# Performance work log

Hardware: AMD Instinct MI355X
Metric: run time of the kernel (lower is better)

## Reference

```python
import jax, jax.numpy as jnp
import numpy as np

D = 512
H = 8
DH = D // H


def setup_inputs() -> dict:
    key = jax.random.key(0)
    ks = jax.random.split(key, 6)
    B, S = 2, 4096
    scale = 1.0 / np.sqrt(D)
    x = jax.random.normal(ks[0], (B, S, D), dtype=jnp.float32)
    W_q = jax.random.normal(ks[1], (D, D), dtype=jnp.float32) * scale
    W_k = jax.random.normal(ks[2], (D, D), dtype=jnp.float32) * scale
    W_v = jax.random.normal(ks[3], (D, D), dtype=jnp.float32) * scale
    W_proj = jax.random.normal(ks[4], (D, D), dtype=jnp.float32) * scale
    b_proj = jax.random.normal(ks[5], (D,), dtype=jnp.float32) * 0.01
    return {"x": x, "W_q": W_q, "W_k": W_k, "W_v": W_v,
            "W_proj": W_proj, "b_proj": b_proj}


def reference(x, W_q, W_k, W_v, W_proj, b_proj):
    B, S, _ = x.shape
    # torch Linear: y = x @ W.T
    def proj(W):
        y = jnp.einsum('bsd,ed->bse', x, W)
        return y.reshape(B, S, H, DH).transpose(0, 2, 1, 3)  # [B,H,S,DH]
    q, k, v = proj(W_q), proj(W_k), proj(W_v)
    scores = jnp.einsum('bhqd,bhkd->bhqk', q, k) / np.sqrt(DH)  # [B,H,S,S]
    causal = jnp.tril(jnp.ones((S, S), dtype=bool))
    neg = jnp.finfo(scores.dtype).min
    scores = jnp.where(causal[None, None, :, :], scores, neg)
    w = jax.nn.softmax(scores, axis=-1)
    attn = jnp.einsum('bhqk,bhkd->bhqd', w, v)  # [B,H,S,DH]
    attn = attn.transpose(0, 2, 1, 3).reshape(B, S, D)
    return jnp.einsum('bsd,ed->bse', attn, W_proj) + b_proj
```

## Files before the change

### kernel.cpp

```cpp
#include <hip/hip_runtime.h>
#include <hip/hip_bf16.h>
#include <stdint.h>

#define D_MODEL 512
#define NH 8
#define DH 64
#define SEQ 4096
#define NBH 16
#define NX  (2 * SEQ * D_MODEL)
#define NW  (D_MODEL * D_MODEL)

typedef __attribute__((ext_vector_type(8))) short bf16x8;
typedef __attribute__((ext_vector_type(4))) float f32x4;
typedef __attribute__((ext_vector_type(16))) float f32x16;

#define CSCALE 0.18033688011112042f

__device__ __forceinline__ uint32_t pkbf(float a, float b) {
    uint32_t r;
    asm("v_cvt_pk_bf16_f32 %0, %1, %2" : "=v"(r) : "v"(a), "v"(b));
    return r;
}

#define SWZ(R) (((R) + ((R) >> 2)) & 3)

#define BAR() do {                                          \
    asm volatile("s_waitcnt lgkmcnt(0)" ::: "memory");      \
    __builtin_amdgcn_s_barrier();                           \
} while (0)

#define BARV() do {                                              \
    asm volatile("s_waitcnt vmcnt(0) lgkmcnt(0)" ::: "memory");  \
    __builtin_amdgcn_s_barrier();                                \
} while (0)

typedef const __attribute__((address_space(1))) void* gvp;
typedef __attribute__((address_space(3))) void* lvp;
__device__ __forceinline__ void gload16(const short* g, short* l) {
    __builtin_amdgcn_global_load_lds((gvp)g, (lvp)l, 16, 0, 0);
}

__device__ __forceinline__ bf16x8 cvt8(float4 u, float4 v, float s) {
    union { uint32_t w[4]; bf16x8 h; } r;
    r.w[0] = pkbf(u.x * s, u.y * s); r.w[1] = pkbf(u.z * s, u.w * s);
    r.w[2] = pkbf(v.x * s, v.y * s); r.w[3] = pkbf(v.z * s, v.w * s);
    return r.h;
}

__global__ __launch_bounds__(256) void cvt_pre(
    const float* __restrict__ x,
    const float* __restrict__ Wq, const float* __restrict__ Wk,
    const float* __restrict__ Wv, const float* __restrict__ Wp,
    short* __restrict__ xb, short* __restrict__ Wb)
{
    const size_t t = ((size_t)blockIdx.x * 256 + threadIdx.x) * 8;
    const float* src; short* dst; float s = 1.0f; size_t off;
    if (t < NX) {
        src = x; dst = xb; off = t;
    } else {
        const size_t u = t - NX;
        const int w = (int)(u >> 18);
        off = u & (NW - 1);
        src = (w == 0) ? Wq : (w == 1) ? Wk : (w == 2) ? Wv : Wp;
        dst = Wb + ((size_t)w << 18);
        s = (w == 0) ? CSCALE : 1.0f;
    }
    float4 a = *(const float4*)(src + off);
    float4 b = *(const float4*)(src + off + 4);
    *(bf16x8*)(dst + off) = cvt8(a, b, s);
}

__global__ __launch_bounds__(256) void qkv_kernel(
    const short* __restrict__ xb, const short* __restrict__ Wb,
    short* __restrict__ Qb, short* __restrict__ Kb, short* __restrict__ Vt)
{
    __shared__ __align__(16) short at[2][4096];
    __shared__ __align__(16) short bt[2][4096];

    const int tid  = threadIdx.x;
    const int wave = tid >> 6;
    const int lane = tid & 63;
    const int ln = lane & 15, quad = lane >> 4;
    const int z = blockIdx.z;
    const short* W = Wb + ((size_t)z << 18);
    const int m0 = blockIdx.x * 128;
    const int n0 = blockIdx.y * 128;
    const int mh = (wave & 1) * 64, nh = (wave >> 1) * 64;

    const int ck0 = tid, ck1 = tid + 256;
    const int R0 = ck0 >> 2, R1 = ck1 >> 2;
    const int c0 = (ck0 & 3) ^ SWZ(R0), c1 = (ck1 & 3) ^ SWZ(R1);
    const int lbase = (tid & 192) * 8;

    auto stage = [&](int buf, int kc) {
        const short* gA0 = xb + (size_t)(m0 + R0) * D_MODEL + kc + c0 * 8;
        const short* gA1 = xb + (size_t)(m0 + R1) * D_MODEL + kc + c1 * 8;
        const short* gB0 = W + (size_t)(n0 + R0) * D_MODEL + kc + c0 * 8;
        const short* gB1 = W + (size_t)(n0 + R1) * D_MODEL + kc + c1 * 8;
        gload16(gA0, &at[buf][lbase]);
        gload16(gA1, &at[buf][lbase] + 2048);
        gload16(gB0, &bt[buf][lbase]);
        gload16(gB1, &bt[buf][lbase] + 2048);
    };

    f32x4 acc[4][4] = {};

    stage(0, 0);

    for (int s = 0; s < 16; ++s) {
        const int cur = s & 1;
        BARV();
        if (s < 15) stage(cur ^ 1, (s + 1) * 32);

        bf16x8 a[4], b[4];
#pragma unroll
        for (int i = 0; i < 4; ++i) {
            const int R = mh + i * 16 + ln;
            a[i] = *(const bf16x8*)(&at[cur][R * 32 + ((quad ^ SWZ(R)) * 8)]);
        }
#pragma unroll
        for (int j = 0; j < 4; ++j) {
            const int R = nh + j * 16 + ln;
            b[j] = *(const bf16x8*)(&bt[cur][R * 32 + ((quad ^ SWZ(R)) * 8)]);
        }
        __builtin_amdgcn_s_setprio(1);
#pragma unroll
        for (int i = 0; i < 4; ++i)
#pragma unroll
            for (int j = 0; j < 4; ++j)
                acc[i][j] = __builtin_amdgcn_mfma_f32_16x16x32_bf16(
                    a[i], b[j], acc[i][j], 0, 0, 0);
        __builtin_amdgcn_s_setprio(0);
    }

    if (z == 2) {
#pragma unroll
        for (int i = 0; i < 4; ++i) {
            const int row0 = m0 + mh + i * 16 + quad * 4;
            const int bb = row0 >> 12, sq = row0 & (SEQ - 1);
#pragma unroll
            for (int j = 0; j < 4; ++j) {
                const int n = n0 + nh + j * 16 + ln;
                const int h = n >> 6, dh = n & 63;
                uint2 st;
                st.x = pkbf(acc[i][j][0], acc[i][j][1]);
                st.y = pkbf(acc[i][j][2], acc[i][j][3]);
                *(uint2*)(Vt + (size_t)((bb * NH + h) * DH + dh) * SEQ + sq) = st;
            }
        }
    } else {
        short* P = (z == 0) ? Qb : Kb;
#pragma unroll
        for (int i = 0; i < 4; ++i)
#pragma unroll
            for (int j = 0; j < 4; ++j) {
                const int n = n0 + nh + j * 16 + ln;
                const int h = n >> 6, dh = n & 63;
                const uint32_t lo = pkbf(acc[i][j][0], acc[i][j][1]);
                const uint32_t hi2 = pkbf(acc[i][j][2], acc[i][j][3]);
#pragma unroll
                for (int r = 0; r < 4; ++r) {
                    const int row = m0 + mh + i * 16 + quad * 4 + r;
                    const int bb = row >> 12, sq = row & (SEQ - 1);
                    const uint32_t w = (r < 2) ? lo : hi2;
                    P[((size_t)((bb * NH + h) * SEQ + sq) << 6) + dh] =
                        (short)((r & 1) ? (w >> 16) : (w & 0xffff));
                }
            }
    }
}

__global__ __launch_bounds__(256) void attn_kernel(
    const short* __restrict__ Qb, const short* __restrict__ Kb,
    const short* __restrict__ Vt, short* __restrict__ ao)
{
    __shared__ __align__(16) short kt[2][4096];
    __shared__ __align__(16) short vt[2][4096];

    const int tid  = threadIdx.x;
    const int wave = tid >> 6;
    const int lane = tid & 63;
    const int l31 = lane & 31, hi = lane >> 5;
    const int bh = blockIdx.y;
    const int w_ = (blockIdx.x + 4 * bh) & 31;
    const int g2 = ((bh >> 3) & 1) ? (31 - w_) : w_;
    const short* Qp = Qb + (size_t)bh * SEQ * DH;
    const short* Kp = Kb + (size_t)bh * SEQ * DH;
    const short* Vp = Vt + (size_t)bh * DH * SEQ;
    const int bb = bh >> 3, h = bh & 7;
    const int q0 = g2 * 128 + wave * 32;
    const int myq = q0 + l31;
    const int jdiag = q0 >> 6;
    const int jmax = 2 * g2 + 1;

    const int ckA = tid, ckB = tid + 256;
    const int RA = ckA >> 3, RB = ckB >> 3;
    const int cA = (ckA & 7) ^ (RA & 7), cB = (ckB & 7) ^ (RB & 7);
    const int RA31 = RA & 31, RB31 = RB & 31;
    const int kkA = (RA & 32) + ((RA31 & 8) << 1) + ((RA31 & 4) << 1)
                  + ((RA31 & 16) >> 2) + (RA31 & 3);
    const int kkB = (RB & 32) + ((RB31 & 8) << 1) + ((RB31 & 4) << 1)
                  + ((RB31 & 16) >> 2) + (RB31 & 3);
    const size_t kOffA = ((size_t)kkA << 6) + cA * 8;
    const size_t kOffB = ((size_t)kkB << 6) + cB * 8;
    const size_t vOffA = (size_t)RA * SEQ + cA * 8;
    const size_t vOffB = (size_t)RB * SEQ + cB * 8;

    bf16x8 sk0, sk1, sv0, sv1;
    auto load_tile = [&](int j) {
        const size_t k0 = (size_t)j * 64;
        sk0 = *(const bf16x8*)(Kp + (k0 << 6) + kOffA);
        sk1 = *(const bf16x8*)(Kp + (k0 << 6) + kOffB);
        sv0 = *(const bf16x8*)(Vp + vOffA + k0);
        sv1 = *(const bf16x8*)(Vp + vOffB + k0);
    };
    auto write_tile = [&](int buf) {
        *(bf16x8*)&kt[buf][ckA * 8] = sk0;
        *(bf16x8*)&kt[buf][ckB * 8] = sk1;
        *(bf16x8*)&vt[buf][ckA * 8] = sv0;
        *(bf16x8*)&vt[buf][ckB * 8] = sv1;
    };

    bf16x8 qf[4];
#pragma unroll
    for (int c = 0; c < 4; ++c)
        qf[c] = *(const bf16x8*)(Qp + (size_t)myq * DH + c * 16 + hi * 8);

    const bf16x8 ones = { (short)0x3F80, (short)0x3F80, (short)0x3F80,
                          (short)0x3F80, (short)0x3F80, (short)0x3F80,
                          (short)0x3F80, (short)0x3F80 };

    f32x16 o0 = {}, o1 = {};
    f32x16 lacc = {};

    load_tile(0);
    write_tile(0);
    load_tile(1);
    BAR();

    for (int j = 0; j <= jmax; ++j) {
        const int cur = j & 1;
        if (j < jmax) {
            write_tile(cur ^ 1);
            if (j + 1 < jmax) load_tile(j + 2);
        }

        if ((j << 6) <= q0 + 31) {
            f32x16 s0 = {}, s1 = {};
            const int sw = l31 & 7;
            __builtin_amdgcn_s_setprio(1);
#pragma unroll
            for (int c = 0; c < 4; ++c) {
                const int pc = ((2 * c + hi) ^ sw) * 8;
                bf16x8 a0 = *(const bf16x8*)(&kt[cur][l31 * 64 + pc]);
                bf16x8 a1 = *(const bf16x8*)(&kt[cur][(32 + l31) * 64 + pc]);
                s0 = __builtin_amdgcn_mfma_f32_32x32x16_bf16(a0, qf[c], s0, 0, 0, 0);
                s1 = __builtin_amdgcn_mfma_f32_32x32x16_bf16(a1, qf[c], s1, 0, 0, 0);
            }
            __builtin_amdgcn_s_setprio(0);
            if (j >= jdiag) {
                const int k0 = j * 64;
#pragma unroll
                for (int reg = 0; reg < 16; ++reg) {
                    const int kl = ((reg >> 2) & 1) * 16 + hi * 8
                                 + ((reg >> 3) & 1) * 4 + (reg & 3);
                    if (k0 + kl > myq)      s0[reg] = -3e38f;
                    if (k0 + 32 + kl > myq) s1[reg] = -3e38f;
                }
            }
#pragma unroll
            for (int i = 0; i < 16; ++i) {
                s0[i] = __builtin_amdgcn_exp2f(s0[i]);
                s1[i] = __builtin_amdgcn_exp2f(s1[i]);
            }

            union { uint32_t u[4]; bf16x8 v; } p00, p01, p10, p11;
            p00.u[0] = pkbf(s0[0], s0[1]);   p00.u[1] = pkbf(s0[2], s0[3]);
            p00.u[2] = pkbf(s0[8], s0[9]);   p00.u[3] = pkbf(s0[10], s0[11]);
            p01.u[0] = pkbf(s0[4], s0[5]);   p01.u[1] = pkbf(s0[6], s0[7]);
            p01.u[2] = pkbf(s0[12], s0[13]); p01.u[3] = pkbf(s0[14], s0[15]);
            p10.u[0] = pkbf(s1[0], s1[1]);   p10.u[1] = pkbf(s1[2], s1[3]);
            p10.u[2] = pkbf(s1[8], s1[9]);   p10.u[3] = pkbf(s1[10], s1[11]);
            p11.u[0] = pkbf(s1[4], s1[5]);   p11.u[1] = pkbf(s1[6], s1[7]);
            p11.u[2] = pkbf(s1[12], s1[13]); p11.u[3] = pkbf(s1[14], s1[15]);

            __builtin_amdgcn_s_setprio(1);
            lacc = __builtin_amdgcn_mfma_f32_32x32x16_bf16(ones, p00.v, lacc, 0, 0, 0);
            lacc = __builtin_amdgcn_mfma_f32_32x32x16_bf16(ones, p01.v, lacc, 0, 0, 0);
            lacc = __builtin_amdgcn_mfma_f32_32x32x16_bf16(ones, p10.v, lacc, 0, 0, 0);
            lacc = __builtin_amdgcn_mfma_f32_32x32x16_bf16(ones, p11.v, lacc, 0, 0, 0);

            {
                const short* vrow = &vt[cur][l31 * 64];
                bf16x8 v00 = *(const bf16x8*)(vrow + (((0 + hi) ^ sw) * 8));
                bf16x8 v01 = *(const bf16x8*)(vrow + (((2 + hi) ^ sw) * 8));
                bf16x8 v10 = *(const bf16x8*)(vrow + (((4 + hi) ^ sw) * 8));
                bf16x8 v11 = *(const bf16x8*)(vrow + (((6 + hi) ^ sw) * 8));
                o0 = __builtin_amdgcn_mfma_f32_32x32x16_bf16(v00, p00.v, o0, 0, 0, 0);
                o0 = __builtin_amdgcn_mfma_f32_32x32x16_bf16(v01, p01.v, o0, 0, 0, 0);
                o0 = __builtin_amdgcn_mfma_f32_32x32x16_bf16(v10, p10.v, o0, 0, 0, 0);
                o0 = __builtin_amdgcn_mfma_f32_32x32x16_bf16(v11, p11.v, o0, 0, 0, 0);
            }
            {
                const short* vrow = &vt[cur][(32 + l31) * 64];
                bf16x8 v00 = *(const bf16x8*)(vrow + (((0 + hi) ^ sw) * 8));
                bf16x8 v01 = *(const bf16x8*)(vrow + (((2 + hi) ^ sw) * 8));
                bf16x8 v10 = *(const bf16x8*)(vrow + (((4 + hi) ^ sw) * 8));
                bf16x8 v11 = *(const bf16x8*)(vrow + (((6 + hi) ^ sw) * 8));
                o1 = __builtin_amdgcn_mfma_f32_32x32x16_bf16(v00, p00.v, o1, 0, 0, 0);
                o1 = __builtin_amdgcn_mfma_f32_32x32x16_bf16(v01, p01.v, o1, 0, 0, 0);
                o1 = __builtin_amdgcn_mfma_f32_32x32x16_bf16(v10, p10.v, o1, 0, 0, 0);
                o1 = __builtin_amdgcn_mfma_f32_32x32x16_bf16(v11, p11.v, o1, 0, 0, 0);
            }
            __builtin_amdgcn_s_setprio(0);
        }
        BAR();
    }
    const float inv = 1.0f / lacc[0];
    short* orow = ao + (size_t)(bb * SEQ + myq) * D_MODEL + h * DH;
#pragma unroll
    for (int c = 0; c < 4; ++c) {
        uint2 st;
        st.x = pkbf(o0[4 * c] * inv,     o0[4 * c + 1] * inv);
        st.y = pkbf(o0[4 * c + 2] * inv, o0[4 * c + 3] * inv);
        *(uint2*)(orow + 8 * c + 4 * hi) = st;
    }
#pragma unroll
    for (int c = 0; c < 4; ++c) {
        uint2 st;
        st.x = pkbf(o1[4 * c] * inv,     o1[4 * c + 1] * inv);
        st.y = pkbf(o1[4 * c + 2] * inv, o1[4 * c + 3] * inv);
        *(uint2*)(orow + 32 + 8 * c + 4 * hi) = st;
    }
}

__global__ __launch_bounds__(256) void proj_kernel(
    const short* __restrict__ attn, const short* __restrict__ Wpb,
    const float* __restrict__ bias, float* __restrict__ out)
{
    __shared__ __align__(16) short at[2][2048];
    __shared__ __align__(16) short bt[2][4096];

    const int tid  = threadIdx.x;
    const int wave = tid >> 6;
    const int lane = tid & 63;
    const int ln = lane & 15, quad = lane >> 4;
    const int m0 = blockIdx.x * 64;
    const int n0 = blockIdx.y * 128;
    const int mh = (wave & 1) * 32, nh = (wave >> 1) * 64;

    const int RA = tid >> 2, cAc = (tid & 3) ^ SWZ(RA);
    const int ck0 = tid, ck1 = tid + 256;
    const int R0 = ck0 >> 2, R1 = ck1 >> 2;
    const int c0 = (ck0 & 3) ^ SWZ(R0), c1 = (ck1 & 3) ^ SWZ(R1);
    const int lbase = (tid & 192) * 8;

    auto stage = [&](int buf, int kc) {
        const short* gA = attn + (size_t)(m0 + RA) * D_MODEL + kc + cAc * 8;
        const short* gB0 = Wpb + (size_t)(n0 + R0) * D_MODEL + kc + c0 * 8;
        const short* gB1 = Wpb + (size_t)(n0 + R1) * D_MODEL + kc + c1 * 8;
        gload16(gA, &at[buf][lbase]);
        gload16(gB0, &bt[buf][lbase]);
        gload16(gB1, &bt[buf][lbase] + 2048);
    };

    f32x4 acc[2][4] = {};

    stage(0, 0);

    for (int s = 0; s < 16; ++s) {
        const int cur = s & 1;
        BARV();
        if (s < 15) stage(cur ^ 1, (s + 1) * 32);

        bf16x8 a[2], b[4];
#pragma unroll
        for (int i = 0; i < 2; ++i) {
            const int R = mh + i * 16 + ln;
            a[i] = *(const bf16x8*)(&at[cur][R * 32 + ((quad ^ SWZ(R)) * 8)]);
        }
#pragma unroll
        for (int j = 0; j < 4; ++j) {
            const int R = nh + j * 16 + ln;
            b[j] = *(const bf16x8*)(&bt[cur][R * 32 + ((quad ^ SWZ(R)) * 8)]);
        }
        __builtin_amdgcn_s_setprio(1);
#pragma unroll
        for (int i = 0; i < 2; ++i)
#pragma unroll
            for (int j = 0; j < 4; ++j)
                acc[i][j] = __builtin_amdgcn_mfma_f32_16x16x32_bf16(
                    a[i], b[j], acc[i][j], 0, 0, 0);
        __builtin_amdgcn_s_setprio(0);
    }
#pragma unroll
    for (int j = 0; j < 4; ++j) {
        const int n = n0 + nh + j * 16 + ln;
        const float bv = bias[n];
#pragma unroll
        for (int i = 0; i < 2; ++i)
#pragma unroll
            for (int r = 0; r < 4; ++r) {
                const int row = m0 + mh + i * 16 + quad * 4 + r;
                out[(size_t)row * D_MODEL + n] = acc[i][j][r] + bv;
            }
    }
}

extern "C" void kernel_launch(void* const* d_in, const int* in_sizes, int n_in,
                              void* d_out, int out_size, void* d_ws, size_t ws_size,
                              hipStream_t stream) {
    const float* x  = (const float*)d_in[0];
    const float* Wq = (const float*)d_in[1];
    const float* Wk = (const float*)d_in[2];
    const float* Wv = (const float*)d_in[3];
    const float* Wp = (const float*)d_in[4];
    const float* bp = (const float*)d_in[5];
    float* out = (float*)d_out;

    short* Qb = (short*)d_ws;
    short* Kb = Qb + (size_t)NBH * SEQ * DH;
    short* Vt = Kb + (size_t)NBH * SEQ * DH;
    short* ab = Vt + (size_t)NBH * SEQ * DH;
    short* Wb = ab + (size_t)NBH * SEQ * DH;

    short* xb = (short*)d_out;

    cvt_pre<<<dim3((NX + 4 * NW) / (8 * 256)), 256, 0, stream>>>(
        x, Wq, Wk, Wv, Wp, xb, Wb);
    qkv_kernel<<<dim3(64, 4, 3), 256, 0, stream>>>(xb, Wb, Qb, Kb, Vt);
    attn_kernel<<<dim3(32, NBH), 256, 0, stream>>>(Qb, Kb, Vt, ab);
    proj_kernel<<<dim3(128, 4), 256, 0, stream>>>(ab, Wb + 3 * (size_t)NW, bp, out);
}
```

Measured before the change: 168.6 us.

## Software-pipeline PV MFMAs across tiles and stage Q/K stores through LDS

The attention loop now defers the P·V and row-sum MFMAs of the previous key tile into the current iteration, so they issue alongside the QK^T MFMAs while the exp and pack of the current tile run afterward. V fragments are loaded into registers before the barrier so the next iteration can use them. Separately, the QKV projection epilogue for Q and K writes the tile into swizzled shared-memory scratch and then emits 16-byte coalesced row stores instead of scattered 2-byte global stores. This raises register pressure, since V and P fragments stay live across iterations, and adds an LDS round trip plus a barrier in the projection kernel.

Measured after the change: 181.2 us. +7.5%, slower.

```diff
diff --git a/kernel.cpp b/kernel.cpp
--- a/kernel.cpp
+++ b/kernel.cpp
@@ -150,23 +150,35 @@
         }
     } else {
         short* P = (z == 0) ? Qb : Kb;
+        BAR();
+        short* scratch = (wave < 2) ? &at[wave][0] : &bt[wave - 2][0];
 #pragma unroll
         for (int i = 0; i < 4; ++i)
 #pragma unroll
             for (int j = 0; j < 4; ++j) {
-                const int n = n0 + nh + j * 16 + ln;
-                const int h = n >> 6, dh = n & 63;
-                const uint32_t lo = pkbf(acc[i][j][0], acc[i][j][1]);
+                const uint32_t lo  = pkbf(acc[i][j][0], acc[i][j][1]);
                 const uint32_t hi2 = pkbf(acc[i][j][2], acc[i][j][3]);
+                const int lc = 16 * j + ln;
+                const int cw = lc & 7, ch = lc >> 3;
 #pragma unroll
                 for (int r = 0; r < 4; ++r) {
-                    const int row = m0 + mh + i * 16 + quad * 4 + r;
-                    const int bb = row >> 12, sq = row & (SEQ - 1);
+                    const int lr = 16 * i + 4 * quad + r;
                     const uint32_t w = (r < 2) ? lo : hi2;
-                    P[((size_t)((bb * NH + h) * SEQ + sq) << 6) + dh] =
+                    scratch[lr * 64 + ((ch ^ (lr & 7)) << 3) + cw] =
                         (short)((r & 1) ? (w >> 16) : (w & 0xffff));
                 }
             }
+        asm volatile("s_waitcnt lgkmcnt(0)" ::: "memory");
+        const int hh = (n0 + nh) >> 6;
+        const int rg = m0 + mh + lane;
+        const int bb2 = rg >> 12, sq2 = rg & (SEQ - 1);
+        short* dst = P + (((size_t)(bb2 * NH + hh) * SEQ + sq2) << 6);
+#pragma unroll
+        for (int c = 0; c < 8; ++c) {
+            const int swc = c ^ (lane & 7);
+            *(bf16x8*)(dst + 8 * c) =
+                *(const bf16x8*)&scratch[lane * 64 + swc * 8];
+        }
     }
 }
 
@@ -233,6 +245,10 @@
     f32x16 o0 = {}, o1 = {};
     f32x16 lacc = {};
 
+    bf16x8 vp0, vp1, vp2, vp3, vp4, vp5, vp6, vp7;
+    bf16x8 pp0, pp1, pp2, pp3;
+    bool havePrev = false;
+
     load_tile(0);
     write_tile(0);
     load_tile(1);
@@ -245,10 +261,12 @@
             if (j + 1 < jmax) load_tile(j + 2);
         }
 
-        if ((j << 6) <= q0 + 31) {
-            f32x16 s0 = {}, s1 = {};
-            const int sw = l31 & 7;
-            __builtin_amdgcn_s_setprio(1);
+        const bool comp = ((j << 6) <= q0 + 31);
+        f32x16 s0 = {}, s1 = {};
+        const int sw = l31 & 7;
+
+        __builtin_amdgcn_s_setprio(1);
+        if (comp) {
 #pragma unroll
             for (int c = 0; c < 4; ++c) {
                 const int pc = ((2 * c + hi) ^ sw) * 8;
@@ -257,7 +275,38 @@
                 s0 = __builtin_amdgcn_mfma_f32_32x32x16_bf16(a0, qf[c], s0, 0, 0, 0);
                 s1 = __builtin_amdgcn_mfma_f32_32x32x16_bf16(a1, qf[c], s1, 0, 0, 0);
             }
-            __builtin_amdgcn_s_setprio(0);
+        }
+        if (havePrev) {
+            lacc = __builtin_amdgcn_mfma_f32_32x32x16_bf16(ones, pp0, lacc, 0, 0, 0);
+            lacc = __builtin_amdgcn_mfma_f32_32x32x16_bf16(ones, pp1, lacc, 0, 0, 0);
+            lacc = __builtin_amdgcn_mfma_f32_32x32x16_bf16(ones, pp2, lacc, 0, 0, 0);
+            lacc = __builtin_amdgcn_mfma_f32_32x32x16_bf16(ones, pp3, lacc, 0, 0, 0);
+            o0 = __builtin_amdgcn_mfma_f32_32x32x16_bf16(vp0, pp0, o0, 0, 0, 0);
+            o0 = __builtin_amdgcn_mfma_f32_32x32x16_bf16(vp1, pp1, o0, 0, 0, 0);
+            o0 = __builtin_amdgcn_mfma_f32_32x32x16_bf16(vp2, pp2, o0, 0, 0, 0);
+            o0 = __builtin_amdgcn_mfma_f32_32x32x16_bf16(vp3, pp3, o0, 0, 0, 0);
+            o1 = __builtin_amdgcn_mfma_f32_32x32x16_bf16(vp4, pp0, o1, 0, 0, 0);
+            o1 = __builtin_amdgcn_mfma_f32_32x32x16_bf16(vp5, pp1, o1, 0, 0, 0);
+            o1 = __builtin_amdgcn_mfma_f32_32x32x16_bf16(vp6, pp2, o1, 0, 0, 0);
+            o1 = __builtin_amdgcn_mfma_f32_32x32x16_bf16(vp7, pp3, o1, 0, 0, 0);
+        }
+        __builtin_amdgcn_s_setprio(0);
+
+        if (comp) {
+            {
+                const short* vrow = &vt[cur][l31 * 64];
+                vp0 = *(const bf16x8*)(vrow + (((0 + hi) ^ sw) * 8));
+                vp1 = *(const bf16x8*)(vrow + (((2 + hi) ^ sw) * 8));
+                vp2 = *(const bf16x8*)(vrow + (((4 + hi) ^ sw) * 8));
+                vp3 = *(const bf16x8*)(vrow + (((6 + hi) ^ sw) * 8));
+            }
+            {
+                const short* vrow = &vt[cur][(32 + l31) * 64];
+                vp4 = *(const bf16x8*)(vrow + (((0 + hi) ^ sw) * 8));
+                vp5 = *(const bf16x8*)(vrow + (((2 + hi) ^ sw) * 8));
+                vp6 = *(const bf16x8*)(vrow + (((4 + hi) ^ sw) * 8));
+                vp7 = *(const bf16x8*)(vrow + (((6 + hi) ^ sw) * 8));
+            }
             if (j >= jdiag) {
                 const int k0 = j * 64;
 #pragma unroll
@@ -273,48 +322,35 @@
                 s0[i] = __builtin_amdgcn_exp2f(s0[i]);
                 s1[i] = __builtin_amdgcn_exp2f(s1[i]);
             }
-
-            union { uint32_t u[4]; bf16x8 v; } p00, p01, p10, p11;
-            p00.u[0] = pkbf(s0[0], s0[1]);   p00.u[1] = pkbf(s0[2], s0[3]);
-            p00.u[2] = pkbf(s0[8], s0[9]);   p00.u[3] = pkbf(s0[10], s0[11]);
-            p01.u[0] = pkbf(s0[4], s0[5]);   p01.u[1] = pkbf(s0[6], s0[7]);
-            p01.u[2] = pkbf(s0[12], s0[13]); p01.u[3] = pkbf(s0[14], s0[15]);
-            p10.u[0] = pkbf(s1[0], s1[1]);   p10.u[1] = pkbf(s1[2], s1[3]);
-            p10.u[2] = pkbf(s1[8], s1[9]);   p10.u[3] = pkbf(s1[10], s1[11]);
-            p11.u[0] = pkbf(s1[4], s1[5]);   p11.u[1] = pkbf(s1[6], s1[7]);
-            p11.u[2] = pkbf(s1[12], s1[13]); p11.u[3] = pkbf(s1[14], s1[15]);
-
-            __builtin_amdgcn_s_setprio(1);
-            lacc = __builtin_amdgcn_mfma_f32_32x32x16_bf16(ones, p00.v, lacc, 0, 0, 0);
-            lacc = __builtin_amdgcn_mfma_f32_32x32x16_bf16(ones, p01.v, lacc, 0, 0, 0);
-            lacc = __builtin_amdgcn_mfma_f32_32x32x16_bf16(ones, p10.v, lacc, 0, 0, 0);
-            lacc = __builtin_amdgcn_mfma_f32_32x32x16_bf16(ones, p11.v, lacc, 0, 0, 0);
-
-            {
-                const short* vrow = &vt[cur][l31 * 64];
-                bf16x8 v00 = *(const bf16x8*)(vrow + (((0 + hi) ^ sw) * 8));
-                bf16x8 v01 = *(const bf16x8*)(vrow + (((2 + hi) ^ sw) * 8));
-                bf16x8 v10 = *(const bf16x8*)(vrow + (((4 + hi) ^ sw) * 8));
-                bf16x8 v11 = *(const bf16x8*)(vrow + (((6 + hi) ^ sw) * 8));
-                o0 = __builtin_amdgcn_mfma_f32_32x32x16_bf16(v00, p00.v, o0, 0, 0, 0);
-                o0 = __builtin_amdgcn_mfma_f32_32x32x16_bf16(v01, p01.v, o0, 0, 0, 0);
-                o0 = __builtin_amdgcn_mfma_f32_32x32x16_bf16(v10, p10.v, o0, 0, 0, 0);
-                o0 = __builtin_amdgcn_mfma_f32_32x32x16_bf16(v11, p11.v, o0, 0, 0, 0);
-            }
-            {
-                const short* vrow = &vt[cur][(32 + l31) * 64];
-                bf16x8 v00 = *(const bf16x8*)(vrow + (((0 + hi) ^ sw) * 8));
-                bf16x8 v01 = *(const bf16x8*)(vrow + (((2 + hi) ^ sw) * 8));
-                bf16x8 v10 = *(const bf16x8*)(vrow + (((4 + hi) ^ sw) * 8));
-                bf16x8 v11 = *(const bf16x8*)(vrow + (((6 + hi) ^ sw) * 8));
-                o1 = __builtin_amdgcn_mfma_f32_32x32x16_bf16(v00, p00.v, o1, 0, 0, 0);
-                o1 = __builtin_amdgcn_mfma_f32_32x32x16_bf16(v01, p01.v, o1, 0, 0, 0);
-                o1 = __builtin_amdgcn_mfma_f32_32x32x16_bf16(v10, p10.v, o1, 0, 0, 0);
-                o1 = __builtin_amdgcn_mfma_f32_32x32x16_bf16(v11, p11.v, o1, 0, 0, 0);
-            }
-            __builtin_amdgcn_s_setprio(0);
-        }
+            union { uint32_t u[4]; bf16x8 v; } P00, P01, P10, P11;
+            P00.u[0] = pkbf(s0[0], s0[1]);   P00.u[1] = pkbf(s0[2], s0[3]);
+            P00.u[2] = pkbf(s0[8], s0[9]);   P00.u[3] = pkbf(s0[10], s0[11]);
+            P01.u[0] = pkbf(s0[4], s0[5]);   P01.u[1] = pkbf(s0[6], s0[7]);
+            P01.u[2] = pkbf(s0[12], s0[13]); P01.u[3] = pkbf(s0[14], s0[15]);
+            P10.u[0] = pkbf(s1[0], s1[1]);   P10.u[1] = pkbf(s1[2], s1[3]);
+            P10.u[2] = pkbf(s1[8], s1[9]);   P10.u[3] = pkbf(s1[10], s1[11]);
+            P11.u[0] = pkbf(s1[4], s1[5]);   P11.u[1] = pkbf(s1[6], s1[7]);
+            P11.u[2] = pkbf(s1[12], s1[13]); P11.u[3] = pkbf(s1[14], s1[15]);
+            pp0 = P00.v; pp1 = P01.v; pp2 = P10.v; pp3 = P11.v;
+        }
+        havePrev = comp;
         BAR();
+    }
+    if (havePrev) {
+        __builtin_amdgcn_s_setprio(1);
+        lacc = __builtin_amdgcn_mfma_f32_32x32x16_bf16(ones, pp0, lacc, 0, 0, 0);
+        lacc = __builtin_amdgcn_mfma_f32_32x32x16_bf16(ones, pp1, lacc, 0, 0, 0);
+        lacc = __builtin_amdgcn_mfma_f32_32x32x16_bf16(ones, pp2, lacc, 0, 0, 0);
+        lacc = __builtin_amdgcn_mfma_f32_32x32x16_bf16(ones, pp3, lacc, 0, 0, 0);
+        o0 = __builtin_amdgcn_mfma_f32_32x32x16_bf16(vp0, pp0, o0, 0, 0, 0);
+        o0 = __builtin_amdgcn_mfma_f32_32x32x16_bf16(vp1, pp1, o0, 0, 0, 0);
+        o0 = __builtin_amdgcn_mfma_f32_32x32x16_bf16(vp2, pp2, o0, 0, 0, 0);
+        o0 = __builtin_amdgcn_mfma_f32_32x32x16_bf16(vp3, pp3, o0, 0, 0, 0);
+        o1 = __builtin_amdgcn_mfma_f32_32x32x16_bf16(vp4, pp0, o1, 0, 0, 0);
+        o1 = __builtin_amdgcn_mfma_f32_32x32x16_bf16(vp5, pp1, o1, 0, 0, 0);
+        o1 = __builtin_amdgcn_mfma_f32_32x32x16_bf16(vp6, pp2, o1, 0, 0, 0);
+        o1 = __builtin_amdgcn_mfma_f32_32x32x16_bf16(vp7, pp3, o1, 0, 0, 0);
+        __builtin_amdgcn_s_setprio(0);
     }
     const float inv = 1.0f / lacc[0];
     short* orow = ao + (size_t)(bb * SEQ + myq) * D_MODEL + h * DH;
```
